# Performance work log

Measured on AMD Instinct MI355X. Metric: run time of the kernel, lower is better.

Reference implementation:

```python
import jax, jax.numpy as jnp
import numpy as np

T = 8192  # sequence length (scan axis)
D = 2048  # channels (independent diagonal SSM states)


def setup_inputs() -> dict:
    key = jax.random.key(0)
    kx, ks, kt = jax.random.split(key, 3)
    x = jax.random.normal(kx, (T, D), dtype=jnp.float32)
    size = jax.random.normal(ks, (D,), dtype=jnp.float32)
    theta = jax.random.normal(kt, (D,), dtype=jnp.float32) * (2.0 * jnp.pi) / 500.0
    return {"x": x, "size": size, "theta": theta}


def reference(x, size, theta):
    # Per-channel complex decay: z_d = exp(-exp(size_d) + i*theta_d)
    z = jnp.exp(-jnp.exp(size) + 1j * theta)  # [D], complex64
    # Linear recurrence v_t = z * v_{t-1} + x_t, solved with a parallel
    # associative scan over pairs (prod, val): combine((pa,va),(pb,vb)) =
    # (pa*pb, va*pb + vb). Vectorized over all D channels at once (the
    # original vmaps a per-channel scan; math is identical).
    P = jnp.broadcast_to(z, x.shape).astype(jnp.complex64)  # [T, D]
    V = x.astype(jnp.complex64)                              # [T, D]

    def combine(a, b):
        pa, va = a
        pb, vb = b
        return (pa * pb, va * pb + vb)

    _, out = jax.lax.associative_scan(combine, (P, V), axis=0)
    return out  # [T, D] complex64
```

## Files before the change

kernel.cpp:

```cpp
#include <hip/hip_runtime.h>

#define T_LEN 8192
#define D_CH  2048
#define C_CHUNKS 64
#define L_CHUNK  (T_LEN / C_CHUNKS)

__device__ __forceinline__ void step_real(float zre, float zim,
                                          float& vre, float& vim, float x) {
    float nre = fmaf(zre, vre, fmaf(-zim, vim, x));
    float nim = fmaf(zre, vim, zim * vre);
    vre = nre; vim = nim;
}

__device__ __forceinline__ void load_z(const float* __restrict__ size_,
                                       const float* __restrict__ theta_,
                                       int d, float& zre, float& zim) {
    float e = expf(size_[d]);
    float r = expf(-e);
    float s, c;
    sincosf(theta_[d], &s, &c);
    zre = r * c;
    zim = r * s;
}

__global__ __launch_bounds__(256) void k_local(const float* __restrict__ x,
                                               const float* __restrict__ size_,
                                               const float* __restrict__ theta_,
                                               float2* __restrict__ b) {
    const int d = blockIdx.x * 256 + threadIdx.x;
    const int c = blockIdx.y;
    float zre, zim;
    load_z(size_, theta_, d, zre, zim);

    const float* xp = x + (size_t)c * L_CHUNK * D_CH + d;
    float vre = 0.f, vim = 0.f;
#pragma unroll 8
    for (int k = 0; k < L_CHUNK; ++k) {
        float xv = xp[(size_t)k * D_CH];
        step_real(zre, zim, vre, vim, xv);
    }
    b[c * D_CH + d] = make_float2(vre, vim);
}

__global__ __launch_bounds__(256) void k_carry(const float* __restrict__ size_,
                                               const float* __restrict__ theta_,
                                               float2* __restrict__ b) {
    const int d = blockIdx.x * 256 + threadIdx.x;
    float e = expf(size_[d]);
    float th = theta_[d];
    float rL = expf(-(float)L_CHUNK * e);
    float sL, cL;
    sincosf((float)L_CHUNK * th, &sL, &cL);
    const float zLre = rL * cL, zLim = rL * sL;

    float cre = 0.f, cim = 0.f;
    for (int base = 0; base < C_CHUNKS; base += 16) {
        float2 loc[16];
#pragma unroll
        for (int j = 0; j < 16; ++j)
            loc[j] = b[(base + j) * D_CH + d];
#pragma unroll
        for (int j = 0; j < 16; ++j) {
            b[(base + j) * D_CH + d] = make_float2(cre, cim);
            float nre = fmaf(zLre, cre, fmaf(-zLim, cim, loc[j].x));
            float nim = fmaf(zLre, cim, fmaf(zLim, cre, loc[j].y));
            cre = nre; cim = nim;
        }
    }
}

template <bool INTERLEAVED>
__global__ __launch_bounds__(256) void k_final(const float* __restrict__ x,
                                               const float* __restrict__ size_,
                                               const float* __restrict__ theta_,
                                               const float2* __restrict__ carry,
                                               float* __restrict__ out) {
    const int d = blockIdx.x * 256 + threadIdx.x;
    const int c = blockIdx.y;
    float zre, zim;
    load_z(size_, theta_, d, zre, zim);

    float2 cv = carry[c * D_CH + d];
    float vre = cv.x, vim = cv.y;
    const float* xp = x + (size_t)c * L_CHUNK * D_CH + d;

    if (INTERLEAVED) {
        float2* outc = (float2*)out;
#pragma unroll 8
        for (int k = 0; k < L_CHUNK; ++k) {
            float xv = xp[(size_t)k * D_CH];
            step_real(zre, zim, vre, vim, xv);
            outc[(size_t)(c * L_CHUNK + k) * D_CH + d] = make_float2(vre, vim);
        }
    } else {
#pragma unroll 8
        for (int k = 0; k < L_CHUNK; ++k) {
            float xv = xp[(size_t)k * D_CH];
            step_real(zre, zim, vre, vim, xv);
            out[(size_t)(c * L_CHUNK + k) * D_CH + d] = vre;
        }
    }
}

extern "C" void kernel_launch(void* const* d_in, const int* in_sizes, int n_in,
                              void* d_out, int out_size, void* d_ws, size_t ws_size,
                              hipStream_t stream) {
    const float* x   = (const float*)d_in[0];
    const float* sz  = (const float*)d_in[1];
    const float* th  = (const float*)d_in[2];
    float2* b = (float2*)d_ws;

    dim3 blk(256);
    dim3 grid1(D_CH / 256, C_CHUNKS);

    k_local<<<grid1, blk, 0, stream>>>(x, sz, th, b);
    k_carry<<<dim3(D_CH / 256), blk, 0, stream>>>(sz, th, b);

    if (out_size == T_LEN * D_CH) {
        k_final<false><<<grid1, blk, 0, stream>>>(x, sz, th, b, (float*)d_out);
    } else {
        k_final<true><<<grid1, blk, 0, stream>>>(x, sz, th, b, (float*)d_out);
    }
}
```

Measured before the change: 134.2 us.

## Process two channels per thread with vector loads and use more time chunks

Each thread now handles two adjacent channels, loading x as float2 and writing output as float2 or float4, so memory accesses are wider. The chunk count becomes a template parameter, and 256 chunks are used when the workspace is large enough, which gives more parallel blocks and shorter serial scans per thread. The carry kernel still works per channel on the same buffer, now read through a float2 view. In exchange, the carry pass must scan a longer chunk chain per channel, and the z values are recomputed per chunk block.

```diff
diff --git a/kernel.cpp b/kernel.cpp
--- a/kernel.cpp
+++ b/kernel.cpp
@@ -2,8 +2,6 @@
 
 #define T_LEN 8192
 #define D_CH  2048
-#define C_CHUNKS 64
-#define L_CHUNK  (T_LEN / C_CHUNKS)
 
 __device__ __forceinline__ void step_real(float zre, float zim,
                                           float& vre, float& vim, float x) {
@@ -23,45 +21,53 @@
     zim = r * s;
 }
 
+template <int CC>
 __global__ __launch_bounds__(256) void k_local(const float* __restrict__ x,
                                                const float* __restrict__ size_,
                                                const float* __restrict__ theta_,
-                                               float2* __restrict__ b) {
-    const int d = blockIdx.x * 256 + threadIdx.x;
-    const int c = blockIdx.y;
-    float zre, zim;
-    load_z(size_, theta_, d, zre, zim);
+                                               float4* __restrict__ b) {
+    constexpr int L = T_LEN / CC;
+    const int dp = blockIdx.x * 256 + threadIdx.x;
+    const int d  = dp * 2;
+    const int c  = blockIdx.y;
 
-    const float* xp = x + (size_t)c * L_CHUNK * D_CH + d;
-    float vre = 0.f, vim = 0.f;
+    float zre0, zim0, zre1, zim1;
+    load_z(size_, theta_, d,     zre0, zim0);
+    load_z(size_, theta_, d + 1, zre1, zim1);
+
+    const float2* xp = (const float2*)x + (size_t)c * L * (D_CH / 2) + dp;
+    float vre0 = 0.f, vim0 = 0.f, vre1 = 0.f, vim1 = 0.f;
 #pragma unroll 8
-    for (int k = 0; k < L_CHUNK; ++k) {
-        float xv = xp[(size_t)k * D_CH];
-        step_real(zre, zim, vre, vim, xv);
+    for (int k = 0; k < L; ++k) {
+        float2 xv = xp[(size_t)k * (D_CH / 2)];
+        step_real(zre0, zim0, vre0, vim0, xv.x);
+        step_real(zre1, zim1, vre1, vim1, xv.y);
     }
-    b[c * D_CH + d] = make_float2(vre, vim);
+    b[c * (D_CH / 2) + dp] = make_float4(vre0, vim0, vre1, vim1);
 }
 
+template <int CC>
 __global__ __launch_bounds__(256) void k_carry(const float* __restrict__ size_,
                                                const float* __restrict__ theta_,
-                                               float2* __restrict__ b) {
+                                               float2* __restrict__ b2) {
+    constexpr int L = T_LEN / CC;
     const int d = blockIdx.x * 256 + threadIdx.x;
-    float e = expf(size_[d]);
+    float e  = expf(size_[d]);
     float th = theta_[d];
-    float rL = expf(-(float)L_CHUNK * e);
+    float rL = expf(-(float)L * e);
     float sL, cL;
-    sincosf((float)L_CHUNK * th, &sL, &cL);
+    sincosf((float)L * th, &sL, &cL);
     const float zLre = rL * cL, zLim = rL * sL;
 
     float cre = 0.f, cim = 0.f;
-    for (int base = 0; base < C_CHUNKS; base += 16) {
+    for (int base = 0; base < CC; base += 16) {
         float2 loc[16];
 #pragma unroll
         for (int j = 0; j < 16; ++j)
-            loc[j] = b[(base + j) * D_CH + d];
+            loc[j] = b2[(base + j) * D_CH + d];
 #pragma unroll
         for (int j = 0; j < 16; ++j) {
-            b[(base + j) * D_CH + d] = make_float2(cre, cim);
+            b2[(base + j) * D_CH + d] = make_float2(cre, cim);
             float nre = fmaf(zLre, cre, fmaf(-zLim, cim, loc[j].x));
             float nim = fmaf(zLre, cim, fmaf(zLim, cre, loc[j].y));
             cre = nre; cim = nim;
@@ -69,56 +75,76 @@
     }
 }
 
-template <bool INTERLEAVED>
+template <int CC, bool INTERLEAVED>
 __global__ __launch_bounds__(256) void k_final(const float* __restrict__ x,
                                                const float* __restrict__ size_,
                                                const float* __restrict__ theta_,
-                                               const float2* __restrict__ carry,
+                                               const float4* __restrict__ carry,
                                                float* __restrict__ out) {
-    const int d = blockIdx.x * 256 + threadIdx.x;
-    const int c = blockIdx.y;
-    float zre, zim;
-    load_z(size_, theta_, d, zre, zim);
+    constexpr int L = T_LEN / CC;
+    const int dp = blockIdx.x * 256 + threadIdx.x;
+    const int d  = dp * 2;
+    const int c  = blockIdx.y;
 
-    float2 cv = carry[c * D_CH + d];
-    float vre = cv.x, vim = cv.y;
-    const float* xp = x + (size_t)c * L_CHUNK * D_CH + d;
+    float zre0, zim0, zre1, zim1;
+    load_z(size_, theta_, d,     zre0, zim0);
+    load_z(size_, theta_, d + 1, zre1, zim1);
+
+    float4 cv = carry[c * (D_CH / 2) + dp];
+    float vre0 = cv.x, vim0 = cv.y, vre1 = cv.z, vim1 = cv.w;
+    const float2* xp = (const float2*)x + (size_t)c * L * (D_CH / 2) + dp;
 
     if (INTERLEAVED) {
-        float2* outc = (float2*)out;
+        float4* o4 = (float4*)out;
 #pragma unroll 8
-        for (int k = 0; k < L_CHUNK; ++k) {
-            float xv = xp[(size_t)k * D_CH];
-            step_real(zre, zim, vre, vim, xv);
-            outc[(size_t)(c * L_CHUNK + k) * D_CH + d] = make_float2(vre, vim);
+        for (int k = 0; k < L; ++k) {
+            float2 xv = xp[(size_t)k * (D_CH / 2)];
+            step_real(zre0, zim0, vre0, vim0, xv.x);
+            step_real(zre1, zim1, vre1, vim1, xv.y);
+            o4[(size_t)(c * L + k) * (D_CH / 2) + dp] =
+                make_float4(vre0, vim0, vre1, vim1);
         }
     } else {
+        float2* o2 = (float2*)out;
 #pragma unroll 8
-        for (int k = 0; k < L_CHUNK; ++k) {
-            float xv = xp[(size_t)k * D_CH];
-            step_real(zre, zim, vre, vim, xv);
-            out[(size_t)(c * L_CHUNK + k) * D_CH + d] = vre;
+        for (int k = 0; k < L; ++k) {
+            float2 xv = xp[(size_t)k * (D_CH / 2)];
+            step_real(zre0, zim0, vre0, vim0, xv.x);
+            step_real(zre1, zim1, vre1, vim1, xv.y);
+            o2[(size_t)(c * L + k) * (D_CH / 2) + dp] = make_float2(vre0, vre1);
         }
+    }
+}
+
+template <int CC>
+static void run_all(const float* x, const float* sz, const float* th,
+                    void* d_out, int out_size, void* d_ws, hipStream_t stream) {
+    float4* b  = (float4*)d_ws;
+    float2* b2 = (float2*)d_ws;
+    dim3 blk(256);
+    dim3 grid1(D_CH / 512, CC);
+
+    k_local<CC><<<grid1, blk, 0, stream>>>(x, sz, th, b);
+    k_carry<CC><<<dim3(D_CH / 256), blk, 0, stream>>>(sz, th, b2);
+
+    if (out_size == T_LEN * D_CH) {
+        k_final<CC, false><<<grid1, blk, 0, stream>>>(x, sz, th, b, (float*)d_out);
+    } else {
+        k_final<CC, true><<<grid1, blk, 0, stream>>>(x, sz, th, b, (float*)d_out);
     }
 }
 
 extern "C" void kernel_launch(void* const* d_in, const int* in_sizes, int n_in,
                               void* d_out, int out_size, void* d_ws, size_t ws_size,
                               hipStream_t stream) {
-    const float* x   = (const float*)d_in[0];
-    const float* sz  = (const float*)d_in[1];
-    const float* th  = (const float*)d_in[2];
-    float2* b = (float2*)d_ws;
+    const float* x  = (const float*)d_in[0];
+    const float* sz = (const float*)d_in[1];
+    const float* th = (const float*)d_in[2];
 
-    dim3 blk(256);
-    dim3 grid1(D_CH / 256, C_CHUNKS);
-
-    k_local<<<grid1, blk, 0, stream>>>(x, sz, th, b);
-    k_carry<<<dim3(D_CH / 256), blk, 0, stream>>>(sz, th, b);
-
-    if (out_size == T_LEN * D_CH) {
-        k_final<false><<<grid1, blk, 0, stream>>>(x, sz, th, b, (float*)d_out);
+    const size_t need256 = (size_t)256 * D_CH * 8;
+    if (ws_size >= need256) {
+        run_all<256>(x, sz, th, d_out, out_size, d_ws, stream);
     } else {
-        k_final<true><<<grid1, blk, 0, stream>>>(x, sz, th, b, (float*)d_out);
+        run_all<64>(x, sz, th, d_out, out_size, d_ws, stream);
     }
 }
```

After: 142.8 us. +6.4%, slower.

## Write local scan directly to output and apply carry correction in a parallel fix pass

Applied to the files above, without the earlier changes.

The local chunk scan now writes its partial results directly into the output, and chunks are doubled to 128. The final pass no longer rescans x sequentially. Instead, a highly parallel fix kernel reads each 16-step tile of output and adds carry times a power of z computed in closed form. This removes the long sequential dependency chain in the final pass at the cost of extra read/write traffic on the output buffer.

```diff
diff --git a/kernel.cpp b/kernel.cpp
--- a/kernel.cpp
+++ b/kernel.cpp
@@ -2,8 +2,8 @@
 
 #define T_LEN 8192
 #define D_CH  2048
-#define C_CHUNKS 64
-#define L_CHUNK  (T_LEN / C_CHUNKS)
+#define CC    128
+#define L_C   (T_LEN / CC)
 
 __device__ __forceinline__ void step_real(float zre, float zim,
                                           float& vre, float& vim, float x) {
@@ -23,45 +23,59 @@
     zim = r * s;
 }
 
-__global__ __launch_bounds__(256) void k_local(const float* __restrict__ x,
-                                               const float* __restrict__ size_,
-                                               const float* __restrict__ theta_,
-                                               float2* __restrict__ b) {
+template <bool ILV>
+__global__ __launch_bounds__(256, 4) void k_local(const float* __restrict__ x,
+                                                  const float* __restrict__ size_,
+                                                  const float* __restrict__ theta_,
+                                                  float* __restrict__ out,
+                                                  float2* __restrict__ ws) {
     const int d = blockIdx.x * 256 + threadIdx.x;
     const int c = blockIdx.y;
     float zre, zim;
     load_z(size_, theta_, d, zre, zim);
 
-    const float* xp = x + (size_t)c * L_CHUNK * D_CH + d;
+    const float* xp = x + (size_t)c * L_C * D_CH + d;
     float vre = 0.f, vim = 0.f;
-#pragma unroll 8
-    for (int k = 0; k < L_CHUNK; ++k) {
-        float xv = xp[(size_t)k * D_CH];
-        step_real(zre, zim, vre, vim, xv);
+    if (ILV) {
+        float2* o2 = (float2*)out + (size_t)c * L_C * D_CH + d;
+#pragma unroll 16
+        for (int k = 0; k < L_C; ++k) {
+            float xv = xp[(size_t)k * D_CH];
+            step_real(zre, zim, vre, vim, xv);
+            o2[(size_t)k * D_CH] = make_float2(vre, vim);
+        }
+    } else {
+        float* o = out + (size_t)c * L_C * D_CH + d;
+#pragma unroll 16
+        for (int k = 0; k < L_C; ++k) {
+            float xv = xp[(size_t)k * D_CH];
+            step_real(zre, zim, vre, vim, xv);
+            o[(size_t)k * D_CH] = vre;
+        }
     }
-    b[c * D_CH + d] = make_float2(vre, vim);
+    ws[c * D_CH + d] = make_float2(vre, vim);
 }
 
 __global__ __launch_bounds__(256) void k_carry(const float* __restrict__ size_,
                                                const float* __restrict__ theta_,
-                                               float2* __restrict__ b) {
+                                               float2* __restrict__ ws) {
     const int d = blockIdx.x * 256 + threadIdx.x;
-    float e = expf(size_[d]);
+    float e  = expf(size_[d]);
     float th = theta_[d];
-    float rL = expf(-(float)L_CHUNK * e);
+    float rL = expf(-(float)L_C * e);
     float sL, cL;
-    sincosf((float)L_CHUNK * th, &sL, &cL);
+    sincosf((float)L_C * th, &sL, &cL);
     const float zLre = rL * cL, zLim = rL * sL;
 
     float cre = 0.f, cim = 0.f;
-    for (int base = 0; base < C_CHUNKS; base += 16) {
+    for (int base = 0; base < CC; base += 16) {
         float2 loc[16];
 #pragma unroll
         for (int j = 0; j < 16; ++j)
-            loc[j] = b[(base + j) * D_CH + d];
+            loc[j] = ws[(base + j) * D_CH + d];
 #pragma unroll
         for (int j = 0; j < 16; ++j) {
-            b[(base + j) * D_CH + d] = make_float2(cre, cim);
+            ws[(base + j) * D_CH + d] = make_float2(cre, cim);
             float nre = fmaf(zLre, cre, fmaf(-zLim, cim, loc[j].x));
             float nim = fmaf(zLre, cim, fmaf(zLim, cre, loc[j].y));
             cre = nre; cim = nim;
@@ -69,35 +83,54 @@
     }
 }
 
-template <bool INTERLEAVED>
-__global__ __launch_bounds__(256) void k_final(const float* __restrict__ x,
-                                               const float* __restrict__ size_,
-                                               const float* __restrict__ theta_,
-                                               const float2* __restrict__ carry,
-                                               float* __restrict__ out) {
-    const int d = blockIdx.x * 256 + threadIdx.x;
-    const int c = blockIdx.y;
-    float zre, zim;
-    load_z(size_, theta_, d, zre, zim);
+template <bool ILV>
+__global__ __launch_bounds__(256, 4) void k_fix(const float* __restrict__ size_,
+                                                const float* __restrict__ theta_,
+                                                const float2* __restrict__ carry,
+                                                float* __restrict__ out) {
+    const int d  = blockIdx.x * 256 + threadIdx.x;
+    const int t0 = blockIdx.y * 16;
+    const int c  = t0 / L_C;
+    const int k0 = t0 % L_C;
 
-    float2 cv = carry[c * D_CH + d];
-    float vre = cv.x, vim = cv.y;
-    const float* xp = x + (size_t)c * L_CHUNK * D_CH + d;
+    float e  = expf(size_[d]);
+    float th = theta_[d];
+    float s, cs;
+    float r1 = expf(-e);
+    sincosf(th, &s, &cs);
+    const float zre = r1 * cs, zim = r1 * s;
+    float p  = (float)(k0 + 1);
+    float rp = expf(-p * e);
+    sincosf(p * th, &s, &cs);
+    float wre = rp * cs, wim = rp * s;
 
-    if (INTERLEAVED) {
-        float2* outc = (float2*)out;
-#pragma unroll 8
-        for (int k = 0; k < L_CHUNK; ++k) {
-            float xv = xp[(size_t)k * D_CH];
-            step_real(zre, zim, vre, vim, xv);
-            outc[(size_t)(c * L_CHUNK + k) * D_CH + d] = make_float2(vre, vim);
+    const float2 cv = carry[c * D_CH + d];
+
+    if (ILV) {
+        float2* o2 = (float2*)out + (size_t)t0 * D_CH + d;
+        float2 loc[16];
+#pragma unroll
+        for (int j = 0; j < 16; ++j) loc[j] = o2[(size_t)j * D_CH];
+#pragma unroll
+        for (int j = 0; j < 16; ++j) {
+            float re = fmaf(wre, cv.x, fmaf(-wim, cv.y, loc[j].x));
+            float im = fmaf(wre, cv.y, fmaf( wim, cv.x, loc[j].y));
+            o2[(size_t)j * D_CH] = make_float2(re, im);
+            float nwre = wre * zre - wim * zim;
+            float nwim = fmaf(wre, zim, wim * zre);
+            wre = nwre; wim = nwim;
         }
     } else {
-#pragma unroll 8
-        for (int k = 0; k < L_CHUNK; ++k) {
-            float xv = xp[(size_t)k * D_CH];
-            step_real(zre, zim, vre, vim, xv);
-            out[(size_t)(c * L_CHUNK + k) * D_CH + d] = vre;
+        float* o = out + (size_t)t0 * D_CH + d;
+        float loc[16];
+#pragma unroll
+        for (int j = 0; j < 16; ++j) loc[j] = o[(size_t)j * D_CH];
+#pragma unroll
+        for (int j = 0; j < 16; ++j) {
+            o[(size_t)j * D_CH] = fmaf(wre, cv.x, fmaf(-wim, cv.y, loc[j]));
+            float nwre = wre * zre - wim * zim;
+            float nwim = fmaf(wre, zim, wim * zre);
+            wre = nwre; wim = nwim;
         }
     }
 }
@@ -105,20 +138,24 @@
 extern "C" void kernel_launch(void* const* d_in, const int* in_sizes, int n_in,
                               void* d_out, int out_size, void* d_ws, size_t ws_size,
                               hipStream_t stream) {
-    const float* x   = (const float*)d_in[0];
-    const float* sz  = (const float*)d_in[1];
-    const float* th  = (const float*)d_in[2];
-    float2* b = (float2*)d_ws;
+    const float* x  = (const float*)d_in[0];
+    const float* sz = (const float*)d_in[1];
+    const float* th = (const float*)d_in[2];
+    float2* ws = (float2*)d_ws;
+    float* out = (float*)d_out;
+    const bool realOnly = (out_size == T_LEN * D_CH);
 
     dim3 blk(256);
-    dim3 grid1(D_CH / 256, C_CHUNKS);
+    dim3 gridL(D_CH / 256, CC);
+    dim3 gridF(D_CH / 256, T_LEN / 16);
 
-    k_local<<<grid1, blk, 0, stream>>>(x, sz, th, b);
-    k_carry<<<dim3(D_CH / 256), blk, 0, stream>>>(sz, th, b);
-
-    if (out_size == T_LEN * D_CH) {
-        k_final<false><<<grid1, blk, 0, stream>>>(x, sz, th, b, (float*)d_out);
+    if (realOnly) {
+        k_local<false><<<gridL, blk, 0, stream>>>(x, sz, th, out, ws);
+        k_carry<<<dim3(D_CH / 256), blk, 0, stream>>>(sz, th, ws);
+        k_fix<false><<<gridF, blk, 0, stream>>>(sz, th, ws, out);
     } else {
-        k_final<true><<<grid1, blk, 0, stream>>>(x, sz, th, b, (float*)d_out);
+        k_local<true><<<gridL, blk, 0, stream>>>(x, sz, th, out, ws);
+        k_carry<<<dim3(D_CH / 256), blk, 0, stream>>>(sz, th, ws);
+        k_fix<true><<<gridF, blk, 0, stream>>>(sz, th, ws, out);
     }
 }
```

Result: slower. 148.7 us (+10.8%).

## Fuse carry propagation into final scan kernel and double chunk count

Applied to the files above, without the earlier changes.

Removes the separate single-row carry kernel. Each final-pass block now recomputes its own incoming carry by folding all preceding chunk sums with z^L. Chunks grow from 64 to 128 for more parallelism and shorter serial loops. Output stores become nontemporal. This trades a serialized low-occupancy launch for redundant per-block carry work that grows linearly with the chunk index.

```diff
diff --git a/kernel.cpp b/kernel.cpp
--- a/kernel.cpp
+++ b/kernel.cpp
@@ -2,8 +2,8 @@
 
 #define T_LEN 8192
 #define D_CH  2048
-#define C_CHUNKS 64
-#define L_CHUNK  (T_LEN / C_CHUNKS)
+#define CC    128
+#define L_C   (T_LEN / CC)
 
 __device__ __forceinline__ void step_real(float zre, float zim,
                                           float& vre, float& vim, float x) {
@@ -23,81 +23,75 @@
     zim = r * s;
 }
 
-__global__ __launch_bounds__(256) void k_local(const float* __restrict__ x,
-                                               const float* __restrict__ size_,
-                                               const float* __restrict__ theta_,
-                                               float2* __restrict__ b) {
+__global__ __launch_bounds__(256) void k_sums(const float* __restrict__ x,
+                                              const float* __restrict__ size_,
+                                              const float* __restrict__ theta_,
+                                              float2* __restrict__ sums) {
     const int d = blockIdx.x * 256 + threadIdx.x;
     const int c = blockIdx.y;
     float zre, zim;
     load_z(size_, theta_, d, zre, zim);
 
-    const float* xp = x + (size_t)c * L_CHUNK * D_CH + d;
+    const float* xp = x + (size_t)c * L_C * D_CH + d;
     float vre = 0.f, vim = 0.f;
-#pragma unroll 8
-    for (int k = 0; k < L_CHUNK; ++k) {
-        float xv = xp[(size_t)k * D_CH];
-        step_real(zre, zim, vre, vim, xv);
-    }
-    b[c * D_CH + d] = make_float2(vre, vim);
+#pragma unroll 16
+    for (int k = 0; k < L_C; ++k)
+        step_real(zre, zim, vre, vim, xp[(size_t)k * D_CH]);
+    sums[c * D_CH + d] = make_float2(vre, vim);
 }
 
-__global__ __launch_bounds__(256) void k_carry(const float* __restrict__ size_,
-                                               const float* __restrict__ theta_,
-                                               float2* __restrict__ b) {
+template <bool ILV>
+__global__ __launch_bounds__(256) void k_scan(const float* __restrict__ x,
+                                              const float* __restrict__ size_,
+                                              const float* __restrict__ theta_,
+                                              const float2* __restrict__ sums,
+                                              float* __restrict__ out) {
     const int d = blockIdx.x * 256 + threadIdx.x;
-    float e = expf(size_[d]);
-    float th = theta_[d];
-    float rL = expf(-(float)L_CHUNK * e);
+    const int c = blockIdx.y;
+
+    float zre, zim;
+    load_z(size_, theta_, d, zre, zim);
+
+    float e  = expf(size_[d]);
+    float rL = expf(-(float)L_C * e);
     float sL, cL;
-    sincosf((float)L_CHUNK * th, &sL, &cL);
+    sincosf((float)L_C * theta_[d], &sL, &cL);
     const float zLre = rL * cL, zLim = rL * sL;
 
     float cre = 0.f, cim = 0.f;
-    for (int base = 0; base < C_CHUNKS; base += 16) {
+    for (int base = 0; base < c; base += 16) {
         float2 loc[16];
 #pragma unroll
         for (int j = 0; j < 16; ++j)
-            loc[j] = b[(base + j) * D_CH + d];
+            loc[j] = (base + j < c) ? sums[(base + j) * D_CH + d]
+                                    : make_float2(0.f, 0.f);
 #pragma unroll
         for (int j = 0; j < 16; ++j) {
-            b[(base + j) * D_CH + d] = make_float2(cre, cim);
-            float nre = fmaf(zLre, cre, fmaf(-zLim, cim, loc[j].x));
-            float nim = fmaf(zLre, cim, fmaf(zLim, cre, loc[j].y));
-            cre = nre; cim = nim;
+            if (base + j < c) {
+                float nre = fmaf(zLre, cre, fmaf(-zLim, cim, loc[j].x));
+                float nim = fmaf(zLre, cim, fmaf(zLim, cre, loc[j].y));
+                cre = nre; cim = nim;
+            }
         }
     }
-}
 
-template <bool INTERLEAVED>
-__global__ __launch_bounds__(256) void k_final(const float* __restrict__ x,
-                                               const float* __restrict__ size_,
-                                               const float* __restrict__ theta_,
-                                               const float2* __restrict__ carry,
-                                               float* __restrict__ out) {
-    const int d = blockIdx.x * 256 + threadIdx.x;
-    const int c = blockIdx.y;
-    float zre, zim;
-    load_z(size_, theta_, d, zre, zim);
-
-    float2 cv = carry[c * D_CH + d];
-    float vre = cv.x, vim = cv.y;
-    const float* xp = x + (size_t)c * L_CHUNK * D_CH + d;
-
-    if (INTERLEAVED) {
-        float2* outc = (float2*)out;
-#pragma unroll 8
-        for (int k = 0; k < L_CHUNK; ++k) {
-            float xv = xp[(size_t)k * D_CH];
-            step_real(zre, zim, vre, vim, xv);
-            outc[(size_t)(c * L_CHUNK + k) * D_CH + d] = make_float2(vre, vim);
+    float vre = cre, vim = cim;
+    const float* xp = x + (size_t)c * L_C * D_CH + d;
+    if (ILV) {
+        float2* o2 = (float2*)out + (size_t)c * L_C * D_CH + d;
+#pragma unroll 16
+        for (int k = 0; k < L_C; ++k) {
+            step_real(zre, zim, vre, vim, xp[(size_t)k * D_CH]);
+            float2 v = make_float2(vre, vim);
+            __builtin_nontemporal_store(v.x, &o2[(size_t)k * D_CH].x);
+            __builtin_nontemporal_store(v.y, &o2[(size_t)k * D_CH].y);
         }
     } else {
-#pragma unroll 8
-        for (int k = 0; k < L_CHUNK; ++k) {
-            float xv = xp[(size_t)k * D_CH];
-            step_real(zre, zim, vre, vim, xv);
-            out[(size_t)(c * L_CHUNK + k) * D_CH + d] = vre;
+        float* o = out + (size_t)c * L_C * D_CH + d;
+#pragma unroll 16
+        for (int k = 0; k < L_C; ++k) {
+            step_real(zre, zim, vre, vim, xp[(size_t)k * D_CH]);
+            __builtin_nontemporal_store(vre, &o[(size_t)k * D_CH]);
         }
     }
 }
@@ -105,20 +99,19 @@
 extern "C" void kernel_launch(void* const* d_in, const int* in_sizes, int n_in,
                               void* d_out, int out_size, void* d_ws, size_t ws_size,
                               hipStream_t stream) {
-    const float* x   = (const float*)d_in[0];
-    const float* sz  = (const float*)d_in[1];
-    const float* th  = (const float*)d_in[2];
-    float2* b = (float2*)d_ws;
+    const float* x  = (const float*)d_in[0];
+    const float* sz = (const float*)d_in[1];
+    const float* th = (const float*)d_in[2];
+    float2* sums = (float2*)d_ws;
+    float* out = (float*)d_out;
+    const bool realOnly = (out_size == T_LEN * D_CH);
 
     dim3 blk(256);
-    dim3 grid1(D_CH / 256, C_CHUNKS);
+    dim3 grid(D_CH / 256, CC);
 
-    k_local<<<grid1, blk, 0, stream>>>(x, sz, th, b);
-    k_carry<<<dim3(D_CH / 256), blk, 0, stream>>>(sz, th, b);
-
-    if (out_size == T_LEN * D_CH) {
-        k_final<false><<<grid1, blk, 0, stream>>>(x, sz, th, b, (float*)d_out);
-    } else {
-        k_final<true><<<grid1, blk, 0, stream>>>(x, sz, th, b, (float*)d_out);
-    }
+    k_sums<<<grid, blk, 0, stream>>>(x, sz, th, sums);
+    if (realOnly)
+        k_scan<false><<<grid, blk, 0, stream>>>(x, sz, th, sums, out);
+    else
+        k_scan<true><<<grid, blk, 0, stream>>>(x, sz, th, sums, out);
 }
```

After: 128.4 us. 1.04x faster.
